# Kernel optimization log

Measured on AMD Instinct MI355X. Metric: run time of the kernel, lower is better.

## Reference

```python
import math
import jax, jax.numpy as jnp
import numpy as np

P_NEW = 10000  # module init: new=10000


def _design_filter(p_full=10000, q_full=48000, L=10, beta=5.0):
    """Octave-style anti-alias FIR: kaiser-windowed sinc, normalized to sum 1
    (the module stores window = h / sum(h))."""
    g = math.gcd(p_full, q_full)
    p, q = p_full // g, q_full // g          # 5, 24
    order = 2 * L * max(p, q)                # 480 -> 481 taps (odd)
    t = np.arange(-order // 2, order // 2 + 1)
    cutoff = 1.0 / (2 * max(p, q))           # normalized cycles/sample
    h = 2 * cutoff * np.sinc(2 * cutoff * t) * np.kaiser(order + 1, beta)
    h = h / np.sum(h)
    return h.astype(np.float32)


def setup_inputs() -> dict:
    key = jax.random.key(0)
    B, T = 32, 1440000  # 32 channels, 30 s @ 48 kHz
    x = jax.random.normal(key, (B, T), dtype=jnp.float32)
    h = jnp.asarray(_design_filter())  # [481]
    return {"x": x, "h": h, "orig_fs": 48000}


def reference(x, h, orig_fs):
    # resample_poly: upsample by `up` (zero-insert), FIR filter, decimate by `down`
    up, down = P_NEW, int(orig_fs)
    g = math.gcd(up, down)
    up //= g
    down //= g                                   # 5, 24 for 48 kHz
    if up == 1 and down == 1:
        return x

    half_len = (h.shape[0] - 1) // 2
    h = h * up                                   # gain compensation
    n_in = x.shape[-1]

    n_pre_pad = (down - half_len % down) % down
    h_padded = jnp.pad(h, (n_pre_pad, 0))
    filt_len = h_padded.shape[0]
    h_flipped = jnp.flip(h_padded)[None, None, :]  # OIH

    x_flat = x.reshape(-1, 1, n_in)                # NCH
    # lhs_dilation=up == zero-stuffed upsample; torch pads filt_len-1 both sides
    # and the torch x_up carries (up-1) trailing zeros -> extra right pad.
    # window_strides=down == the y[..., ::down] decimation, computed without waste.
    y_down = jax.lax.conv_general_dilated(
        x_flat, h_flipped,
        window_strides=(down,),
        padding=[(filt_len - 1, filt_len - 1 + up - 1)],
        lhs_dilation=(up,),
        dimension_numbers=("NCH", "OIH", "NCH"),
    )

    n_out = n_in * up // down + (1 if (n_in * up) % down else 0)
    n_pre_remove = (half_len + n_pre_pad) // down
    y = y_down[..., n_pre_remove:n_pre_remove + n_out]
    return y.reshape(x.shape[:-1] + (n_out,))
```

## Files before the change

### kernel.cpp

```cpp
#include <hip/hip_runtime.h>


#define NIN    1440000
#define NOUTR  300000
#define NROWS  32
#define KTOT   60000
#define NCHUNK 938
#define TILE_E 1632
#define TILE_P 1648
#define NT8    204

typedef __attribute__((ext_vector_type(8))) short short8v;
typedef __attribute__((ext_vector_type(4))) float float4v;

__device__ __forceinline__ unsigned short f2b(float f) {
    unsigned u = __builtin_bit_cast(unsigned, f);
    u += 0x7fff + ((u >> 16) & 1);
    return (unsigned short)(u >> 16);
}

__global__ void prep_taps_kernel(const float* __restrict__ h,
                                 unsigned short* __restrict__ Bpk) {
    int i = blockIdx.x * blockDim.x + threadIdx.x;
    if (i < 2048) {
        int j = i & 7, l = (i >> 3) & 63, m = i >> 9;
        int d = l & 15, q = l >> 4;
        int c = 32 * m + 8 * q + j;
        int t = 24 * d + 480 - 5 * c;
        float v = (d < 5 && t >= 0 && t <= 480) ? h[t] * 5.0f : 0.0f;
        Bpk[i] = f2b(v);
    }
}

__global__ __launch_bounds__(256, 7) void resample_kernel(
    const float* __restrict__ x, const unsigned short* __restrict__ Bpk,
    float* __restrict__ y)
{
    __shared__ short ldsb[TILE_P];
    const int tid  = threadIdx.x;
    const int lane = tid & 63;
    const int wv   = tid >> 6;
    const int row  = blockIdx.y;
    const int ct   = blockIdx.x;
    const float* __restrict__ xr = x + (size_t)row * NIN;
    const int g0 = 1536 * ct - 48;

    const short8v B0 = *reinterpret_cast<const short8v*>(Bpk + (0 * 64 + lane) * 8);
    const short8v B1 = *reinterpret_cast<const short8v*>(Bpk + (1 * 64 + lane) * 8);
    const short8v B2 = *reinterpret_cast<const short8v*>(Bpk + (2 * 64 + lane) * 8);
    const short8v B3 = *reinterpret_cast<const short8v*>(Bpk + (3 * 64 + lane) * 8);

    if (tid < TILE_P - TILE_E) ldsb[TILE_E + tid] = 0;

    if (tid < NT8) {
        float4 pa, pb;
        if (g0 >= 0 && g0 + TILE_E <= NIN) {
            const float4* __restrict__ p = reinterpret_cast<const float4*>(xr + g0);
            pa = p[2 * tid];
            pb = p[2 * tid + 1];
        } else {
            float v[8];
            #pragma unroll
            for (int j = 0; j < 8; ++j) {
                const int g = g0 + 8 * tid + j;
                v[j] = ((unsigned)g < NIN) ? xr[g] : 0.0f;
            }
            pa = make_float4(v[0], v[1], v[2], v[3]);
            pb = make_float4(v[4], v[5], v[6], v[7]);
        }
        unsigned r0, r1, r2, r3;
        asm("v_cvt_pk_bf16_f32 %0, %1, %2" : "=v"(r0) : "v"(pa.x), "v"(pa.y));
        asm("v_cvt_pk_bf16_f32 %0, %1, %2" : "=v"(r1) : "v"(pa.z), "v"(pa.w));
        asm("v_cvt_pk_bf16_f32 %0, %1, %2" : "=v"(r2) : "v"(pb.x), "v"(pb.y));
        asm("v_cvt_pk_bf16_f32 %0, %1, %2" : "=v"(r3) : "v"(pb.z), "v"(pb.w));
        *reinterpret_cast<uint4*>(&ldsb[8 * tid]) = make_uint4(r0, r1, r2, r3);
    }
    __syncthreads();

    const int r = lane & 15, q = lane >> 4;
    const short* __restrict__ ap = &ldsb[24 * (16 * wv + r) + 8 * q];
    const short8v A0 = *reinterpret_cast<const short8v*>(ap);
    const short8v A1 = *reinterpret_cast<const short8v*>(ap + 32);
    const short8v A2 = *reinterpret_cast<const short8v*>(ap + 64);
    const short8v A3 = *reinterpret_cast<const short8v*>(ap + 96);

    float4v acc = {0.f, 0.f, 0.f, 0.f};
    acc = __builtin_amdgcn_mfma_f32_16x16x32_bf16(A0, B0, acc, 0, 0, 0);
    acc = __builtin_amdgcn_mfma_f32_16x16x32_bf16(A1, B1, acc, 0, 0, 0);
    acc = __builtin_amdgcn_mfma_f32_16x16x32_bf16(A2, B2, acc, 0, 0, 0);
    acc = __builtin_amdgcn_mfma_f32_16x16x32_bf16(A3, B3, acc, 0, 0, 0);

    const int d = lane & 15;
    if (d < 5) {
        const int kbase = 64 * ct + 16 * wv + 4 * q;
        float* __restrict__ yr = y + (size_t)row * NOUTR;
        #pragma unroll
        for (int j = 0; j < 4; ++j) {
            const int k = kbase + j;
            if (k < KTOT) yr[5 * (size_t)k + d] = acc[j];
        }
    }
}

extern "C" void kernel_launch(void* const* d_in, const int* in_sizes, int n_in,
                              void* d_out, int out_size, void* d_ws, size_t ws_size,
                              hipStream_t stream) {
    const float* x = (const float*)d_in[0];
    const float* h = (const float*)d_in[1];
    float* y = (float*)d_out;
    unsigned short* Bpk = (unsigned short*)d_ws;

    prep_taps_kernel<<<8, 256, 0, stream>>>(h, Bpk);
    dim3 grid(NCHUNK, NROWS);
    resample_kernel<<<grid, 256, 0, stream>>>(x, Bpk, y);
}
```

Measured before the change: 48.70 us.

## Pack three output phases per MFMA column and loop blocks over chunks

The tap matrix is repacked so each MFMA uses 15 of its 16 columns (three output groups of five phases) with K=192, where before only 5 of 16 columns did useful work. Each block now walks up to four chunks serially, staging a larger bf16 tile per chunk, so fewer blocks are launched and fewer tap fragments are loaded per output. The cost is more LDS and registers per block, lower occupancy, and serial load-then-compute steps inside a block with no overlap between them.

After: 41.63 us (median of 2 runs). -14.5%, faster.

```diff
diff --git a/kernel.cpp b/kernel.cpp
--- a/kernel.cpp
+++ b/kernel.cpp
@@ -5,10 +5,12 @@
 #define NOUTR  300000
 #define NROWS  32
 #define KTOT   60000
-#define NCHUNK 938
-#define TILE_E 1632
-#define TILE_P 1648
-#define NT8    204
+#define KB     192
+#define GENS   313
+#define S      4
+#define NBX    79
+#define TILE_E 4752
+#define NU8    594
 
 typedef __attribute__((ext_vector_type(8))) short short8v;
 typedef __attribute__((ext_vector_type(4))) float float4v;
@@ -22,82 +24,96 @@
 __global__ void prep_taps_kernel(const float* __restrict__ h,
                                  unsigned short* __restrict__ Bpk) {
     int i = blockIdx.x * blockDim.x + threadIdx.x;
-    if (i < 2048) {
+    if (i < 3072) {
         int j = i & 7, l = (i >> 3) & 63, m = i >> 9;
-        int d = l & 15, q = l >> 4;
+        int col = l & 15, q = l >> 4;
         int c = 32 * m + 8 * q + j;
-        int t = 24 * d + 480 - 5 * c;
-        float v = (d < 5 && t >= 0 && t <= 480) ? h[t] * 5.0f : 0.0f;
+        int D = col / 5, d = col - 5 * D;
+        int t = 24 * d + 480 - 5 * (c - 24 * D);
+        float v = (col < 15 && t >= 0 && t <= 480) ? h[t] * 5.0f : 0.0f;
         Bpk[i] = f2b(v);
     }
 }
 
-__global__ __launch_bounds__(256, 7) void resample_kernel(
+__global__ __launch_bounds__(256, 5) void resample_kernel(
     const float* __restrict__ x, const unsigned short* __restrict__ Bpk,
     float* __restrict__ y)
 {
-    __shared__ short ldsb[TILE_P];
+    __shared__ __align__(16) short ldsb[TILE_E];
     const int tid  = threadIdx.x;
     const int lane = tid & 63;
     const int wv   = tid >> 6;
     const int row  = blockIdx.y;
-    const int ct   = blockIdx.x;
+    const int gb   = blockIdx.x * S;
+    const int n    = min(S, GENS - gb);
     const float* __restrict__ xr = x + (size_t)row * NIN;
-    const int g0 = 1536 * ct - 48;
 
-    const short8v B0 = *reinterpret_cast<const short8v*>(Bpk + (0 * 64 + lane) * 8);
-    const short8v B1 = *reinterpret_cast<const short8v*>(Bpk + (1 * 64 + lane) * 8);
-    const short8v B2 = *reinterpret_cast<const short8v*>(Bpk + (2 * 64 + lane) * 8);
-    const short8v B3 = *reinterpret_cast<const short8v*>(Bpk + (3 * 64 + lane) * 8);
+    short8v Bf[6];
+    #pragma unroll
+    for (int m = 0; m < 6; ++m)
+        Bf[m] = *reinterpret_cast<const short8v*>(Bpk + (m * 64 + lane) * 8);
 
-    if (tid < TILE_P - TILE_E) ldsb[TILE_E + tid] = 0;
+    const int q = lane >> 4, r = lane & 15;
+    const int col = r;
+    const int D = col / 5, d = col - 5 * D;
+    const int aoff = 1152 * wv + 72 * r + 8 * q;
 
-    if (tid < NT8) {
-        float4 pa, pb;
-        if (g0 >= 0 && g0 + TILE_E <= NIN) {
-            const float4* __restrict__ p = reinterpret_cast<const float4*>(xr + g0);
-            pa = p[2 * tid];
-            pb = p[2 * tid + 1];
+    for (int s = 0; s < n; ++s) {
+        const int kgen = KB * (gb + s);
+        const int gg = 24 * kgen - 48;
+        __syncthreads();
+
+        if (gg >= 0 && gg + TILE_E <= NIN) {
+            const float4* __restrict__ p = reinterpret_cast<const float4*>(xr + gg);
+            auto stu = [&](int u) {
+                const float4 pa = p[2 * u], pb = p[2 * u + 1];
+                unsigned r0, r1, r2, r3;
+                asm("v_cvt_pk_bf16_f32 %0, %1, %2" : "=v"(r0) : "v"(pa.x), "v"(pa.y));
+                asm("v_cvt_pk_bf16_f32 %0, %1, %2" : "=v"(r1) : "v"(pa.z), "v"(pa.w));
+                asm("v_cvt_pk_bf16_f32 %0, %1, %2" : "=v"(r2) : "v"(pb.x), "v"(pb.y));
+                asm("v_cvt_pk_bf16_f32 %0, %1, %2" : "=v"(r3) : "v"(pb.z), "v"(pb.w));
+                *reinterpret_cast<uint4*>(&ldsb[8 * u]) = make_uint4(r0, r1, r2, r3);
+            };
+            stu(tid);
+            stu(tid + 256);
+            if (tid < NU8 - 512) stu(tid + 512);
         } else {
-            float v[8];
+            auto stu = [&](int u) {
+                float v[8];
+                #pragma unroll
+                for (int j = 0; j < 8; ++j) {
+                    const int g = gg + 8 * u + j;
+                    v[j] = ((unsigned)g < NIN) ? xr[g] : 0.0f;
+                }
+                unsigned r0, r1, r2, r3;
+                asm("v_cvt_pk_bf16_f32 %0, %1, %2" : "=v"(r0) : "v"(v[0]), "v"(v[1]));
+                asm("v_cvt_pk_bf16_f32 %0, %1, %2" : "=v"(r1) : "v"(v[2]), "v"(v[3]));
+                asm("v_cvt_pk_bf16_f32 %0, %1, %2" : "=v"(r2) : "v"(v[4]), "v"(v[5]));
+                asm("v_cvt_pk_bf16_f32 %0, %1, %2" : "=v"(r3) : "v"(v[6]), "v"(v[7]));
+                *reinterpret_cast<uint4*>(&ldsb[8 * u]) = make_uint4(r0, r1, r2, r3);
+            };
+            stu(tid);
+            stu(tid + 256);
+            if (tid < NU8 - 512) stu(tid + 512);
+        }
+        __syncthreads();
+
+        const short* __restrict__ ap = &ldsb[aoff];
+        float4v acc = {0.f, 0.f, 0.f, 0.f};
+        #pragma unroll
+        for (int m = 0; m < 6; ++m) {
+            const short8v A = *reinterpret_cast<const short8v*>(ap + 32 * m);
+            acc = __builtin_amdgcn_mfma_f32_16x16x32_bf16(A, Bf[m], acc, 0, 0, 0);
+        }
+
+        if (col < 15) {
+            const int kw = kgen + 48 * wv + 12 * q + D;
+            float* __restrict__ yr = y + (size_t)row * NOUTR;
             #pragma unroll
-            for (int j = 0; j < 8; ++j) {
-                const int g = g0 + 8 * tid + j;
-                v[j] = ((unsigned)g < NIN) ? xr[g] : 0.0f;
+            for (int jj = 0; jj < 4; ++jj) {
+                const int k = kw + 3 * jj;
+                if (k < KTOT) yr[5 * (size_t)k + d] = acc[jj];
             }
-            pa = make_float4(v[0], v[1], v[2], v[3]);
-            pb = make_float4(v[4], v[5], v[6], v[7]);
-        }
-        unsigned r0, r1, r2, r3;
-        asm("v_cvt_pk_bf16_f32 %0, %1, %2" : "=v"(r0) : "v"(pa.x), "v"(pa.y));
-        asm("v_cvt_pk_bf16_f32 %0, %1, %2" : "=v"(r1) : "v"(pa.z), "v"(pa.w));
-        asm("v_cvt_pk_bf16_f32 %0, %1, %2" : "=v"(r2) : "v"(pb.x), "v"(pb.y));
-        asm("v_cvt_pk_bf16_f32 %0, %1, %2" : "=v"(r3) : "v"(pb.z), "v"(pb.w));
-        *reinterpret_cast<uint4*>(&ldsb[8 * tid]) = make_uint4(r0, r1, r2, r3);
-    }
-    __syncthreads();
-
-    const int r = lane & 15, q = lane >> 4;
-    const short* __restrict__ ap = &ldsb[24 * (16 * wv + r) + 8 * q];
-    const short8v A0 = *reinterpret_cast<const short8v*>(ap);
-    const short8v A1 = *reinterpret_cast<const short8v*>(ap + 32);
-    const short8v A2 = *reinterpret_cast<const short8v*>(ap + 64);
-    const short8v A3 = *reinterpret_cast<const short8v*>(ap + 96);
-
-    float4v acc = {0.f, 0.f, 0.f, 0.f};
-    acc = __builtin_amdgcn_mfma_f32_16x16x32_bf16(A0, B0, acc, 0, 0, 0);
-    acc = __builtin_amdgcn_mfma_f32_16x16x32_bf16(A1, B1, acc, 0, 0, 0);
-    acc = __builtin_amdgcn_mfma_f32_16x16x32_bf16(A2, B2, acc, 0, 0, 0);
-    acc = __builtin_amdgcn_mfma_f32_16x16x32_bf16(A3, B3, acc, 0, 0, 0);
-
-    const int d = lane & 15;
-    if (d < 5) {
-        const int kbase = 64 * ct + 16 * wv + 4 * q;
-        float* __restrict__ yr = y + (size_t)row * NOUTR;
-        #pragma unroll
-        for (int j = 0; j < 4; ++j) {
-            const int k = kbase + j;
-            if (k < KTOT) yr[5 * (size_t)k + d] = acc[j];
         }
     }
 }
@@ -110,7 +126,7 @@
     float* y = (float*)d_out;
     unsigned short* Bpk = (unsigned short*)d_ws;
 
-    prep_taps_kernel<<<8, 256, 0, stream>>>(h, Bpk);
-    dim3 grid(NCHUNK, NROWS);
+    prep_taps_kernel<<<12, 256, 0, stream>>>(h, Bpk);
+    dim3 grid(NBX, NROWS);
     resample_kernel<<<grid, 256, 0, stream>>>(x, Bpk, y);
 }
```
